# Performance work log

Hardware: AMD Instinct MI355X
Metric: run time of the kernel (lower is better)

## Reference

```python
import jax, jax.numpy as jnp
import numpy as np

L = 4      # number of layers (graph nodes)
B = 128    # batch
H = 4096   # neurons per layer


def setup_inputs() -> dict:
    key = jax.random.key(0)
    k1, k2, k3 = jax.random.split(key, 3)
    # per-layer source activations, stacked: [L, B, H]
    states = jax.random.normal(k1, (L, B, H), dtype=jnp.float32)
    # all Connection weight matrices, W[t, s] maps source s -> target t: [L, L, H_out, H_in]
    # scaled by 1/sqrt(H) so summed matmuls stay O(1) (original uses constant w_init)
    W = jax.random.normal(k2, (L, L, H, H), dtype=jnp.float32) * (1.0 / np.sqrt(H))
    # external inputs added into each target's current: [L, B, H]
    ext = jax.random.normal(k3, (L, B, H), dtype=jnp.float32)
    return {"states": states, "W": W, "ext": ext}


def reference(states, W, ext):
    # Synapses/Links: for each target t, sum over sources s of (x_s @ W[t,s].T)
    # (Connection.forward is x @ w.T). Single fused einsum replaces the
    # jit.fork fan-out over L*L small matmuls + Python-level sum.
    currents = jnp.einsum('sbh,tsoh->tbo', states, W) + ext  # [L, B, H]
    # Layer/Neurons: per-node activation function
    return jnp.tanh(currents)
```

## Files before the change

kernel.cpp:

```cpp
#include <hip/hip_runtime.h>
#include <hip/hip_bf16.h>
#include <stdint.h>

#define L_ 4
#define B_ 128
#define H_ 4096
#define BK 64
#define BN 32
#define KIT 256
#define NTHR 256
#define ABYTES (128*BK*2)
#define WBYTES (BN*BK*2)
#define BUFB   (ABYTES+WBYTES)

typedef _Float16 f16x8 __attribute__((ext_vector_type(8)));
typedef float    f32x4 __attribute__((ext_vector_type(4)));
typedef float    f4    __attribute__((ext_vector_type(4)));
typedef uint32_t u32x4 __attribute__((ext_vector_type(4)));
typedef uint32_t u32x2 __attribute__((ext_vector_type(2)));

__device__ __forceinline__ uint32_t pack2(float a, float b) {
  const _Float16 ha = (_Float16)a;
  const _Float16 hb = (_Float16)b;
  const uint32_t ua = (uint32_t)__builtin_bit_cast(uint16_t, ha);
  const uint32_t ub = (uint32_t)__builtin_bit_cast(uint16_t, hb);
  return ua | (ub << 16);
}

__global__ void cvt_states_kernel(const float* __restrict__ x,
                                  uint32_t* __restrict__ y, int n4) {
  const int i = blockIdx.x * blockDim.x + threadIdx.x;
  if (i < n4) {
    f4 v = reinterpret_cast<const f4*>(x)[i];
    u32x2 o;
    o.x = pack2(v.x, v.y);
    o.y = pack2(v.z, v.w);
    reinterpret_cast<u32x2*>(y)[i] = o;
  }
}

__device__ __forceinline__ void gld_lds16(const void* g, void* l) {
  __builtin_amdgcn_global_load_lds(
      (const __attribute__((address_space(1))) void*)g,
      (__attribute__((address_space(3))) void*)l, 16, 0, 0);
}

#define BAR_VM(N_) do {                                          \
    __builtin_amdgcn_sched_barrier(0);                           \
    asm volatile("s_waitcnt vmcnt(" #N_ ") lgkmcnt(0)" ::: "memory"); \
    __builtin_amdgcn_sched_barrier(0);                           \
    __builtin_amdgcn_s_barrier();                                \
    __builtin_amdgcn_sched_barrier(0);                           \
  } while (0)

__global__ __launch_bounds__(NTHR, 2)
void net_gemm_kernel(const uint16_t* __restrict__ statesh,
                     const float* __restrict__ Wm,
                     const float* __restrict__ ext,
                     float* __restrict__ out)
{
  __shared__ __align__(16) uint8_t lds[3 * BUFB];

  const int tid  = threadIdx.x;
  const int bid  = blockIdx.x;
  const int t    = bid >> 7;
  const int n0   = (bid & 127) * BN;

  const int wv   = tid >> 6;
  const int lane = tid & 63;
  const int lid  = lane & 15;
  const int lh   = lane >> 4;

  uint32_t a_src[4];
  #pragma unroll
  for (int j = 0; j < 4; ++j) {
    const uint32_t row = (uint32_t)(j * 32 + wv * 8 + (lane >> 3));
    const uint32_t cb  = (uint32_t)(lane & 7) * 16;
    a_src[j] = row * (H_ * 2) + (cb ^ ((row & 7) << 4));
  }

  const int wrow = tid >> 4;
  const int wcol = (tid & 15) * 4;
  const float* w_base = Wm + ((size_t)t * L_ * H_ + (size_t)(n0 + wrow)) * H_ + wcol;
  const uint32_t w_st0 =
      (uint32_t)ABYTES + (uint32_t)wrow * 128 + (((uint32_t)(tid & 15) * 8) ^ ((uint32_t)(wrow & 7) << 4));
  const uint32_t w_st1 = w_st0 + 16 * 128;

  uint32_t a_rd[2][2], b_rd[2][2];
  #pragma unroll
  for (int mf = 0; mf < 2; ++mf)
    #pragma unroll
    for (int kk = 0; kk < 2; ++kk) {
      const int row = wv * 32 + mf * 16 + lid;
      a_rd[mf][kk] = (uint32_t)row * 128 +
                     (((uint32_t)(kk * 64 + lh * 16)) ^ ((uint32_t)(lid & 7) << 4));
    }
  #pragma unroll
  for (int nf = 0; nf < 2; ++nf)
    #pragma unroll
    for (int kk = 0; kk < 2; ++kk) {
      const int row = nf * 16 + lid;
      b_rd[nf][kk] = (uint32_t)ABYTES + (uint32_t)row * 128 +
                     (((uint32_t)(kk * 64 + lh * 16)) ^ ((uint32_t)(lid & 7) << 4));
    }

  f32x4 acc[2][2] = {};
  f4 wf[2][4];

  auto LOADW = [&](int kidx, f4 (&w)[4]) {
    const int s  = kidx >> 6;
    const int h0 = (kidx & 63) << 6;
    const float* wp = w_base + (size_t)s * ((size_t)H_ * H_) + h0;
    w[0] = __builtin_nontemporal_load(reinterpret_cast<const f4*>(wp));
    w[1] = __builtin_nontemporal_load(reinterpret_cast<const f4*>(wp + 16 * (size_t)H_));
    w[2] = w[0];
    w[3] = w[1];
  };

  auto ALDS = [&](int kidx, int bufi) {
    const uint8_t* g = (const uint8_t*)statesh +
                       (size_t)(kidx >> 6) * (B_ * H_ * 2) + (size_t)(kidx & 63) * 128;
    uint8_t* l = lds + bufi * BUFB + wv * 1024;
    #pragma unroll
    for (int j = 0; j < 4; ++j)
      gld_lds16(g + a_src[j], l + j * 4096);
  };

  auto WRITEW = [&](int bufi, f4 (&w)[4]) {
    uint8_t* base = lds + bufi * BUFB;
    u32x2 w0, w1;
    w0.x = pack2(w[0].x, w[0].y); w0.y = pack2(w[0].z, w[0].w);
    w1.x = pack2(w[1].x, w[1].y); w1.y = pack2(w[1].z, w[1].w);
    *reinterpret_cast<u32x2*>(base + w_st0) = w0;
    *reinterpret_cast<u32x2*>(base + w_st1) = w1;
  };

  auto COMPUTE = [&](int bufi) {
    const uint8_t* base = lds + bufi * BUFB;
    f16x8 av[2][2], bv[2][2];
    #pragma unroll
    for (int mf = 0; mf < 2; ++mf)
      #pragma unroll
      for (int kk = 0; kk < 2; ++kk)
        av[mf][kk] = *reinterpret_cast<const f16x8*>(base + a_rd[mf][kk]);
    #pragma unroll
    for (int nf = 0; nf < 2; ++nf)
      #pragma unroll
      for (int kk = 0; kk < 2; ++kk)
        bv[nf][kk] = *reinterpret_cast<const f16x8*>(base + b_rd[nf][kk]);
    #pragma unroll
    for (int kk = 0; kk < 2; ++kk)
      #pragma unroll
      for (int mf = 0; mf < 2; ++mf)
        #pragma unroll
        for (int nf = 0; nf < 2; ++nf)
          acc[mf][nf] = __builtin_amdgcn_mfma_f32_16x16x32_f16(
              av[mf][kk], bv[nf][kk], acc[mf][nf], 0, 0, 0);
  };

  LOADW(0, wf[0]);
  LOADW(1, wf[1]);
  ALDS(0, 0);
  ALDS(1, 1);
  WRITEW(0, wf[0]);
  BAR_VM(4);

  #define BODY(kk_, C_, N_, WT_, LE_) do {      \
      LOADW((kk_) + 2, wf[LE_]);                \
      ALDS((kk_) + 2, (N_));                    \
      COMPUTE((C_));                            \
      WRITEW((WT_), wf[1 - (LE_)]);             \
      BAR_VM(6);                                \
    } while (0)

  #pragma unroll 1
  for (int k = 0; k < 252; k += 6) {
    BODY(k + 0, 0, 2, 1, 0);
    BODY(k + 1, 1, 0, 2, 1);
    BODY(k + 2, 2, 1, 0, 0);
    BODY(k + 3, 0, 2, 1, 1);
    BODY(k + 4, 1, 0, 2, 0);
    BODY(k + 5, 2, 1, 0, 1);
  }
  BODY(252, 0, 2, 1, 0);
  BODY(253, 1, 0, 2, 1);
  COMPUTE(2);
  WRITEW(0, wf[1]);
  BAR_VM(0);
  COMPUTE(0);
  #undef BODY

  #pragma unroll
  for (int mf = 0; mf < 2; ++mf)
    #pragma unroll
    for (int nf = 0; nf < 2; ++nf)
      #pragma unroll
      for (int j = 0; j < 4; ++j) {
        const int brow = wv * 32 + mf * 16 + lh * 4 + j;
        const int ocol = n0 + nf * 16 + lid;
        const size_t idx = ((size_t)(t * B_ + brow)) * H_ + ocol;
        out[idx] = tanhf(acc[mf][nf][j] + ext[idx]);
      }
}

__global__ __launch_bounds__(NTHR, 2)
void net_gemm_fb(const float* __restrict__ statesf,
                 const float* __restrict__ Wm,
                 const float* __restrict__ ext,
                 float* __restrict__ out)
{
  __shared__ __align__(16) uint8_t lds[2 * BUFB];

  const int tid  = threadIdx.x;
  const int bid  = blockIdx.x;
  const int t    = bid >> 7;
  const int n0   = (bid & 127) * BN;
  const int wv   = tid >> 6;
  const int lane = tid & 63;
  const int lid  = lane & 15;
  const int lh   = lane >> 4;

  const int arow = tid >> 3;
  const int acol = (tid & 7) * 8;
  const uint32_t a_st_off =
      (uint32_t)arow * 128 + (((uint32_t)(tid & 7) * 16) ^ ((uint32_t)(arow & 7) << 4));
  const float* af_base = statesf + (size_t)arow * H_ + acol;

  const int wrow = tid >> 4;
  const int wcol = (tid & 15) * 4;
  const float* w_base = Wm + ((size_t)t * L_ * H_ + (size_t)(n0 + wrow)) * H_ + wcol;
  const uint32_t w_st0 =
      (uint32_t)ABYTES + (uint32_t)wrow * 128 + (((uint32_t)(tid & 15) * 8) ^ ((uint32_t)(wrow & 7) << 4));
  const uint32_t w_st1 = w_st0 + 16 * 128;

  uint32_t a_rd[2][2], b_rd[2][2];
  #pragma unroll
  for (int mf = 0; mf < 2; ++mf)
    #pragma unroll
    for (int kk = 0; kk < 2; ++kk) {
      const int row = wv * 32 + mf * 16 + lid;
      a_rd[mf][kk] = (uint32_t)row * 128 +
                     (((uint32_t)(kk * 64 + lh * 16)) ^ ((uint32_t)(lid & 7) << 4));
    }
  #pragma unroll
  for (int nf = 0; nf < 2; ++nf)
    #pragma unroll
    for (int kk = 0; kk < 2; ++kk) {
      const int row = nf * 16 + lid;
      b_rd[nf][kk] = (uint32_t)ABYTES + (uint32_t)row * 128 +
                     (((uint32_t)(kk * 64 + lh * 16)) ^ ((uint32_t)(lid & 7) << 4));
    }

  f32x4 acc[2][2] = {};
  f4 af0[4][2], af1[4][2], wf0[2], wf1[2];

  auto LOADg = [&](int kidx, f4 (&af)[4][2], f4 (&wfx)[2]) {
    const int s  = kidx >> 6;
    const int h0 = (kidx & 63) << 6;
    const float* ap = af_base + (size_t)s * (B_ * H_) + h0;
    #pragma unroll
    for (int j = 0; j < 4; ++j) {
      af[j][0] = *reinterpret_cast<const f4*>(ap + (size_t)j * (32 * H_));
      af[j][1] = *reinterpret_cast<const f4*>(ap + (size_t)j * (32 * H_) + 4);
    }
    const float* wp = w_base + (size_t)s * ((size_t)H_ * H_) + h0;
    wfx[0] = __builtin_nontemporal_load(reinterpret_cast<const f4*>(wp));
    wfx[1] = __builtin_nontemporal_load(reinterpret_cast<const f4*>(wp + 16 * (size_t)H_));
  };

  auto WRITEg = [&](uint8_t* base, f4 (&af)[4][2], f4 (&wfx)[2]) {
    #pragma unroll
    for (int j = 0; j < 4; ++j) {
      u32x4 v;
      v.x = pack2(af[j][0].x, af[j][0].y);
      v.y = pack2(af[j][0].z, af[j][0].w);
      v.z = pack2(af[j][1].x, af[j][1].y);
      v.w = pack2(af[j][1].z, af[j][1].w);
      *reinterpret_cast<u32x4*>(base + j * 4096 + a_st_off) = v;
    }
    u32x2 w0, w1;
    w0.x = pack2(wfx[0].x, wfx[0].y); w0.y = pack2(wfx[0].z, wfx[0].w);
    w1.x = pack2(wfx[1].x, wfx[1].y); w1.y = pack2(wfx[1].z, wfx[1].w);
    *reinterpret_cast<u32x2*>(base + w_st0) = w0;
    *reinterpret_cast<u32x2*>(base + w_st1) = w1;
  };

  auto COMPUTE = [&](const uint8_t* base) {
    f16x8 av[2][2], bv[2][2];
    #pragma unroll
    for (int mf = 0; mf < 2; ++mf)
      #pragma unroll
      for (int kk = 0; kk < 2; ++kk)
        av[mf][kk] = *reinterpret_cast<const f16x8*>(base + a_rd[mf][kk]);
    #pragma unroll
    for (int nf = 0; nf < 2; ++nf)
      #pragma unroll
      for (int kk = 0; kk < 2; ++kk)
        bv[nf][kk] = *reinterpret_cast<const f16x8*>(base + b_rd[nf][kk]);
    #pragma unroll
    for (int kk = 0; kk < 2; ++kk)
      #pragma unroll
      for (int mf = 0; mf < 2; ++mf)
        #pragma unroll
        for (int nf = 0; nf < 2; ++nf)
          acc[mf][nf] = __builtin_amdgcn_mfma_f32_16x16x32_f16(
              av[mf][kk], bv[nf][kk], acc[mf][nf], 0, 0, 0);
  };

  uint8_t* buf0 = lds;
  uint8_t* buf1 = lds + BUFB;

  LOADg(0, af0, wf0);
  LOADg(1, af1, wf1);
  WRITEg(buf0, af0, wf0);
  BAR_VM(0);

  #pragma unroll 1
  for (int k = 0; k < KIT; k += 2) {
    if (k + 2 < KIT) LOADg(k + 2, af0, wf0);
    COMPUTE(buf0);
    WRITEg(buf1, af1, wf1);
    BAR_VM(0);
    if (k + 3 < KIT) LOADg(k + 3, af1, wf1);
    COMPUTE(buf1);
    if (k + 2 < KIT) {
      WRITEg(buf0, af0, wf0);
      BAR_VM(0);
    }
  }

  #pragma unroll
  for (int mf = 0; mf < 2; ++mf)
    #pragma unroll
    for (int nf = 0; nf < 2; ++nf)
      #pragma unroll
      for (int j = 0; j < 4; ++j) {
        const int brow = wv * 32 + mf * 16 + lh * 4 + j;
        const int ocol = n0 + nf * 16 + lid;
        const size_t idx = ((size_t)(t * B_ + brow)) * H_ + ocol;
        out[idx] = tanhf(acc[mf][nf][j] + ext[idx]);
      }
}

extern "C" void kernel_launch(void* const* d_in, const int* in_sizes, int n_in,
                              void* d_out, int out_size, void* d_ws, size_t ws_size,
                              hipStream_t stream) {
  const float* states = (const float*)d_in[0];
  const float* W      = (const float*)d_in[1];
  const float* ext    = (const float*)d_in[2];
  float* out          = (float*)d_out;

  const size_t nstates = (size_t)L_ * B_ * H_;
  if (ws_size >= nstates * sizeof(uint16_t)) {
    const int n4 = (int)(nstates / 4);
    cvt_states_kernel<<<(n4 + 255) / 256, 256, 0, stream>>>(states, (uint32_t*)d_ws, n4);
    net_gemm_kernel<<<512, NTHR, 0, stream>>>((const uint16_t*)d_ws, W, ext, out);
  } else {
    net_gemm_fb<<<512, NTHR, 0, stream>>>(states, W, ext, out);
  }
}
```

Measured before the change: 265.2 us.

## Split K across two block groups with partial buffers and a reduce kernel

Adds a split-K variant that launches 1024 blocks, each covering half the source layers, writes fp32 partial sums to workspace, and a separate reduce kernel adds partials plus ext and applies tanh. It also replaces the triple-buffered global_load_lds pipeline with register-staged double buffering and plain LDS writes. The goal is more blocks in flight to keep all CUs busy streaming the large W matrix, at the cost of extra partial-sum traffic and an additional kernel launch.

```diff
diff --git a/kernel.cpp b/kernel.cpp
--- a/kernel.cpp
+++ b/kernel.cpp
@@ -7,8 +7,8 @@
 #define H_ 4096
 #define BK 64
 #define BN 32
-#define KIT 256
 #define NTHR 256
+#define NTOT (L_*B_*H_)
 #define ABYTES (128*BK*2)
 #define WBYTES (BN*BK*2)
 #define BUFB   (ABYTES+WBYTES)
@@ -39,45 +39,42 @@
   }
 }
 
-__device__ __forceinline__ void gld_lds16(const void* g, void* l) {
-  __builtin_amdgcn_global_load_lds(
-      (const __attribute__((address_space(1))) void*)g,
-      (__attribute__((address_space(3))) void*)l, 16, 0, 0);
-}
-
-#define BAR_VM(N_) do {                                          \
-    __builtin_amdgcn_sched_barrier(0);                           \
-    asm volatile("s_waitcnt vmcnt(" #N_ ") lgkmcnt(0)" ::: "memory"); \
-    __builtin_amdgcn_sched_barrier(0);                           \
-    __builtin_amdgcn_s_barrier();                                \
-    __builtin_amdgcn_sched_barrier(0);                           \
-  } while (0)
-
-__global__ __launch_bounds__(NTHR, 2)
+__device__ __forceinline__ void bar_lgkm0() {
+  __builtin_amdgcn_sched_barrier(0);
+  asm volatile("s_waitcnt lgkmcnt(0)");
+  __builtin_amdgcn_sched_barrier(0);
+  __builtin_amdgcn_s_barrier();
+  __builtin_amdgcn_sched_barrier(0);
+}
+
+template<int SPLIT>
+__global__ __launch_bounds__(NTHR, 2*SPLIT)
 void net_gemm_kernel(const uint16_t* __restrict__ statesh,
                      const float* __restrict__ Wm,
                      const float* __restrict__ ext,
-                     float* __restrict__ out)
+                     float* __restrict__ out,
+                     float* __restrict__ part)
 {
-  __shared__ __align__(16) uint8_t lds[3 * BUFB];
+  constexpr int KITN = 256 / SPLIT;
+  __shared__ __align__(16) uint8_t lds[2 * BUFB];
 
   const int tid  = threadIdx.x;
   const int bid  = blockIdx.x;
-  const int t    = bid >> 7;
   const int n0   = (bid & 127) * BN;
+  const int t    = (bid >> 7) & 3;
+  const int kh   = bid >> 9;
+  const int sbase = kh * (L_ / SPLIT);
 
   const int wv   = tid >> 6;
   const int lane = tid & 63;
   const int lid  = lane & 15;
   const int lh   = lane >> 4;
 
-  uint32_t a_src[4];
-  #pragma unroll
-  for (int j = 0; j < 4; ++j) {
-    const uint32_t row = (uint32_t)(j * 32 + wv * 8 + (lane >> 3));
-    const uint32_t cb  = (uint32_t)(lane & 7) * 16;
-    a_src[j] = row * (H_ * 2) + (cb ^ ((row & 7) << 4));
-  }
+  const int arow = tid >> 3;
+  const int acol = (tid & 7) * 8;
+  const uint32_t a_st_off =
+      (uint32_t)arow * 128 + (((uint32_t)(tid & 7) * 16) ^ ((uint32_t)(arow & 7) << 4));
+  const uint16_t* ah_base = statesh + (size_t)arow * H_ + acol;
 
   const int wrow = tid >> 4;
   const int wcol = (tid & 15) * 4;
@@ -105,38 +102,34 @@
     }
 
   f32x4 acc[2][2] = {};
-  f4 wf[2][4];
-
-  auto LOADW = [&](int kidx, f4 (&w)[4]) {
-    const int s  = kidx >> 6;
+
+  u32x4 ah0[4], ah1[4];
+  f4    wf0[2], wf1[2];
+
+  auto LOADg = [&](int kidx, u32x4 (&ah)[4], f4 (&wf)[2]) {
+    const int s  = sbase + (kidx >> 6);
     const int h0 = (kidx & 63) << 6;
+    const uint16_t* ap = ah_base + (size_t)s * (B_ * H_) + h0;
+    #pragma unroll
+    for (int j = 0; j < 4; ++j)
+      ah[j] = *reinterpret_cast<const u32x4*>(ap + (size_t)j * (32 * H_));
     const float* wp = w_base + (size_t)s * ((size_t)H_ * H_) + h0;
-    w[0] = __builtin_nontemporal_load(reinterpret_cast<const f4*>(wp));
-    w[1] = __builtin_nontemporal_load(reinterpret_cast<const f4*>(wp + 16 * (size_t)H_));
-    w[2] = w[0];
-    w[3] = w[1];
-  };
-
-  auto ALDS = [&](int kidx, int bufi) {
-    const uint8_t* g = (const uint8_t*)statesh +
-                       (size_t)(kidx >> 6) * (B_ * H_ * 2) + (size_t)(kidx & 63) * 128;
-    uint8_t* l = lds + bufi * BUFB + wv * 1024;
+    wf[0] = __builtin_nontemporal_load(reinterpret_cast<const f4*>(wp));
+    wf[1] = __builtin_nontemporal_load(reinterpret_cast<const f4*>(wp + 16 * (size_t)H_));
+  };
+
+  auto WRITEg = [&](uint8_t* base, u32x4 (&ah)[4], f4 (&wf)[2]) {
     #pragma unroll
     for (int j = 0; j < 4; ++j)
-      gld_lds16(g + a_src[j], l + j * 4096);
-  };
-
-  auto WRITEW = [&](int bufi, f4 (&w)[4]) {
-    uint8_t* base = lds + bufi * BUFB;
+      *reinterpret_cast<u32x4*>(base + j * 4096 + a_st_off) = ah[j];
     u32x2 w0, w1;
-    w0.x = pack2(w[0].x, w[0].y); w0.y = pack2(w[0].z, w[0].w);
-    w1.x = pack2(w[1].x, w[1].y); w1.y = pack2(w[1].z, w[1].w);
+    w0.x = pack2(wf[0].x, wf[0].y); w0.y = pack2(wf[0].z, wf[0].w);
+    w1.x = pack2(wf[1].x, wf[1].y); w1.y = pack2(wf[1].z, wf[1].w);
     *reinterpret_cast<u32x2*>(base + w_st0) = w0;
     *reinterpret_cast<u32x2*>(base + w_st1) = w1;
   };
 
-  auto COMPUTE = [&](int bufi) {
-    const uint8_t* base = lds + bufi * BUFB;
+  auto COMPUTE = [&](const uint8_t* base) {
     f16x8 av[2][2], bv[2][2];
     #pragma unroll
     for (int mf = 0; mf < 2; ++mf)
@@ -158,37 +151,28 @@
               av[mf][kk], bv[nf][kk], acc[mf][nf], 0, 0, 0);
   };
 
-  LOADW(0, wf[0]);
-  LOADW(1, wf[1]);
-  ALDS(0, 0);
-  ALDS(1, 1);
-  WRITEW(0, wf[0]);
-  BAR_VM(4);
-
-  #define BODY(kk_, C_, N_, WT_, LE_) do {      \
-      LOADW((kk_) + 2, wf[LE_]);                \
-      ALDS((kk_) + 2, (N_));                    \
-      COMPUTE((C_));                            \
-      WRITEW((WT_), wf[1 - (LE_)]);             \
-      BAR_VM(6);                                \
-    } while (0)
+  uint8_t* buf0 = lds;
+  uint8_t* buf1 = lds + BUFB;
+
+  LOADg(0, ah0, wf0);
+  LOADg(1, ah1, wf1);
+  WRITEg(buf0, ah0, wf0);
+  bar_lgkm0();
 
   #pragma unroll 1
-  for (int k = 0; k < 252; k += 6) {
-    BODY(k + 0, 0, 2, 1, 0);
-    BODY(k + 1, 1, 0, 2, 1);
-    BODY(k + 2, 2, 1, 0, 0);
-    BODY(k + 3, 0, 2, 1, 1);
-    BODY(k + 4, 1, 0, 2, 0);
-    BODY(k + 5, 2, 1, 0, 1);
+  for (int k = 0; k < KITN; k += 2) {
+    if (k + 2 < KITN) LOADg(k + 2, ah0, wf0);
+    COMPUTE(buf0);
+    WRITEg(buf1, ah1, wf1);
+    bar_lgkm0();
+
+    if (k + 3 < KITN) LOADg(k + 3, ah1, wf1);
+    COMPUTE(buf1);
+    if (k + 2 < KITN) {
+      WRITEg(buf0, ah0, wf0);
+      bar_lgkm0();
+    }
   }
-  BODY(252, 0, 2, 1, 0);
-  BODY(253, 1, 0, 2, 1);
-  COMPUTE(2);
-  WRITEW(0, wf[1]);
-  BAR_VM(0);
-  COMPUTE(0);
-  #undef BODY
 
   #pragma unroll
   for (int mf = 0; mf < 2; ++mf)
@@ -199,8 +183,30 @@
         const int brow = wv * 32 + mf * 16 + lh * 4 + j;
         const int ocol = n0 + nf * 16 + lid;
         const size_t idx = ((size_t)(t * B_ + brow)) * H_ + ocol;
-        out[idx] = tanhf(acc[mf][nf][j] + ext[idx]);
+        if constexpr (SPLIT == 1) {
+          out[idx] = tanhf(acc[mf][nf][j] + ext[idx]);
+        } else {
+          float* pb = part + (size_t)kh * NTOT;
+          __builtin_nontemporal_store(acc[mf][nf][j], &pb[idx]);
+        }
       }
+}
+
+__global__ __launch_bounds__(NTHR)
+void reduce_kernel(const float* __restrict__ part,
+                   const float* __restrict__ ext,
+                   float* __restrict__ out)
+{
+  const int i = blockIdx.x * blockDim.x + threadIdx.x;
+  f4 p0 = __builtin_nontemporal_load(reinterpret_cast<const f4*>(part) + i);
+  f4 p1 = __builtin_nontemporal_load(reinterpret_cast<const f4*>(part + NTOT) + i);
+  f4 e  = reinterpret_cast<const f4*>(ext)[i];
+  f4 r;
+  r.x = tanhf(p0.x + p1.x + e.x);
+  r.y = tanhf(p0.y + p1.y + e.y);
+  r.z = tanhf(p0.z + p1.z + e.z);
+  r.w = tanhf(p0.w + p1.w + e.w);
+  reinterpret_cast<f4*>(out)[i] = r;
 }
 
 __global__ __launch_bounds__(NTHR, 2)
@@ -313,19 +319,19 @@
   LOADg(0, af0, wf0);
   LOADg(1, af1, wf1);
   WRITEg(buf0, af0, wf0);
-  BAR_VM(0);
+  bar_lgkm0();
 
   #pragma unroll 1
-  for (int k = 0; k < KIT; k += 2) {
-    if (k + 2 < KIT) LOADg(k + 2, af0, wf0);
+  for (int k = 0; k < 256; k += 2) {
+    if (k + 2 < 256) LOADg(k + 2, af0, wf0);
     COMPUTE(buf0);
     WRITEg(buf1, af1, wf1);
-    BAR_VM(0);
-    if (k + 3 < KIT) LOADg(k + 3, af1, wf1);
+    bar_lgkm0();
+    if (k + 3 < 256) LOADg(k + 3, af1, wf1);
     COMPUTE(buf1);
-    if (k + 2 < KIT) {
+    if (k + 2 < 256) {
       WRITEg(buf0, af0, wf0);
-      BAR_VM(0);
+      bar_lgkm0();
     }
   }
 
@@ -350,11 +356,20 @@
   const float* ext    = (const float*)d_in[2];
   float* out          = (float*)d_out;
 
-  const size_t nstates = (size_t)L_ * B_ * H_;
-  if (ws_size >= nstates * sizeof(uint16_t)) {
-    const int n4 = (int)(nstates / 4);
-    cvt_states_kernel<<<(n4 + 255) / 256, 256, 0, stream>>>(states, (uint32_t*)d_ws, n4);
-    net_gemm_kernel<<<512, NTHR, 0, stream>>>((const uint16_t*)d_ws, W, ext, out);
+  const size_t st_bytes   = (size_t)NTOT * 2;
+  const size_t part_bytes = (size_t)2 * NTOT * 4;
+  const int n4 = NTOT / 4;
+
+  if (ws_size >= st_bytes + part_bytes) {
+    float* part = (float*)((uint8_t*)d_ws + st_bytes);
+    cvt_states_kernel<<<n4 / 256, NTHR, 0, stream>>>(states, (uint32_t*)d_ws, n4);
+    net_gemm_kernel<2><<<1024, NTHR, 0, stream>>>(
+        (const uint16_t*)d_ws, W, ext, out, part);
+    reduce_kernel<<<n4 / 256, NTHR, 0, stream>>>(part, ext, out);
+  } else if (ws_size >= st_bytes) {
+    cvt_states_kernel<<<n4 / 256, NTHR, 0, stream>>>(states, (uint32_t*)d_ws, n4);
+    net_gemm_kernel<1><<<512, NTHR, 0, stream>>>(
+        (const uint16_t*)d_ws, W, ext, out, nullptr);
   } else {
     net_gemm_fb<<<512, NTHR, 0, stream>>>(states, W, ext, out);
   }
```

Result: faster. 257.1 us (-3.1%).
